# Performance work log

Hardware: AMD Instinct MI355X
Metric: run time of the kernel (lower is better)

Reference implementation:

```python
import jax, jax.numpy as jnp
import numpy as np

L = 3264          # seq_length
K = 12            # ktc=4 -> K=12
LOCC = 4          # ktc=4 -> Locc=4
BLK = 12          # mmse_block_size
DMIN, DMAX = -10, 10  # delay_search_range
RHO = 0.9         # assumed frequency-correlation coefficient for MMSE C matrix


def setup_inputs() -> dict:
    key = jax.random.key(0)
    k1, k2, k3 = jax.random.split(key, 3)
    ls_real = jax.random.normal(k1, (L,), dtype=jnp.float32)
    ls_imag = jax.random.normal(k2, (L,), dtype=jnp.float32)
    cyclic_shifts = jax.random.randint(k3, (8, 4), 0, K, dtype=jnp.int32)
    return {"ls_real": ls_real, "ls_imag": ls_imag, "cyclic_shifts": cyclic_shifts}


def _estimate(ls, cs_flat):
    P = cs_flat.shape[0]  # total ports across all users
    ideal = ((K - cs_flat) % K) * (L // K)                      # [P] ideal CIR peak positions
    h_time = jnp.fft.ifft(ls)
    hmag = jnp.abs(h_time)                                      # [L]
    idx = jnp.arange(L)
    # circular search window [ideal+DMIN, ideal+DMAX] around each ideal peak
    rel = (idx[None, :] - (ideal[:, None] + DMIN)) % L          # [P, L]
    mask = rel <= (DMAX - DMIN)
    vals = jnp.where(mask, hmag[None, :], -jnp.inf)
    peak = jnp.argmax(vals, axis=1)                             # [P]
    d = peak - ideal
    offset = jnp.where((peak > ideal) & (d > L // 2), d - L,
             jnp.where((ideal - peak) > L // 2, d + L, d))
    m = offset + ideal                                          # [P] phasor shift amounts
    # phasor exp(j 2 pi m n / L); reduce m*n mod L to keep fp32 phase accurate
    n = jnp.arange(L)
    phase = (2.0 * np.pi / L) * ((m[:, None] * n[None, :]) % L).astype(jnp.float32)
    phasor = jnp.exp(1j * phase).astype(jnp.complex64)          # [P, L]
    h_up = ls[None, :] * phasor                                 # [P, L]
    # OCC demux: average every LOCC points
    h_avg = h_up.reshape(P, L // LOCC, LOCC).mean(axis=-1)      # [P, L/LOCC]
    # linear interpolation back to L, centers of groups as sample points
    g = LOCC
    orig = (g - 1) / 2.0 + g * jnp.arange(L // g, dtype=jnp.float32)
    new = jnp.arange(L, dtype=jnp.float32)
    interp1 = jax.vmap(lambda r: jnp.interp(new, orig, r))
    h_interp = (interp1(jnp.real(h_avg)) + 1j * interp1(jnp.imag(h_avg))).astype(jnp.complex64)  # [P, L]
    # residual of multi-port reconstruction
    h_recon = jnp.sum(h_interp / phasor, axis=0)
    residual = ls - h_recon
    # noise power from adjacent-tone differences
    diff = ls[1:] - ls[:-1]
    noise_power = jnp.mean(jnp.abs(diff) ** 2) / 2.0
    # add residual back per port
    h_wr = h_interp + residual[None, :] * phasor                # [P, L]
    # block MMSE: h_mmse = C (C + noise I)^{-1} h_block, C[i,j] = rho^{|i-j|}
    ij = jnp.abs(jnp.arange(BLK)[:, None] - jnp.arange(BLK)[None, :])
    C = (RHO ** ij).astype(jnp.float32)
    A = C + noise_power * jnp.eye(BLK, dtype=jnp.float32)
    F = jnp.linalg.solve(A.T, C.T).T                            # F = C @ inv(A), [BLK, BLK]
    blocks = h_wr.reshape(P, L // BLK, BLK)
    h_mmse = jnp.einsum('pbk,jk->pbj', blocks, F.astype(jnp.complex64)).reshape(P, L)
    # the original nested loop emits the same P inner results for each of P outer (u,p)
    return jnp.tile(h_mmse, (P, 1))                             # [P*P, L]


def reference(ls_real, ls_imag, cyclic_shifts):
    ls = (ls_real + 1j * ls_imag).astype(jnp.complex64)
    cs_flat = cyclic_shifts.reshape(-1)
    return _estimate(ls, cs_flat)
```

## Files before the change

kernel.cpp:

```cpp
#include <hip/hip_runtime.h>
#include <math.h>

#define LL    3264
#define KK    12
#define PP    32
#define NW    21
#define DMIN  (-10)
#define GAVG  (LL/4)
#define NBLK  (LL/12)
#define NIDE  12
#define NMAG  (NIDE*NW)

#define OUT_REAL  (PP*PP*LL)
#define OUT_CPLX  (PP*PP*LL*2)
#define SCRATCH_F 270520

__global__ void k_win_noise_F(const float* __restrict__ lsr,
                              const float* __restrict__ lsi,
                              double* __restrict__ mag2,
                              float* __restrict__ F) {
    __shared__ double sre[256], sim[256];
    const int b = blockIdx.x;
    const int tid = threadIdx.x;
    const float c0 = (float)(2.0 * M_PI / (double)LL);
    if (b < NMAG) {
        const int i = b / NW, r = b % NW;
        int t = i * (LL / KK) + DMIN + r;
        t %= LL; if (t < 0) t += LL;
        double are = 0.0, aim = 0.0;
        for (int n = tid; n < LL; n += 256) {
            unsigned mod = (unsigned)(n * t) % LL;
            float ang = c0 * (float)mod;
            float ss, cc;
            sincosf(ang, &ss, &cc);
            float xr = lsr[n], xi = lsi[n];
            are += (double)(xr * cc - xi * ss);
            aim += (double)(xr * ss + xi * cc);
        }
        sre[tid] = are; sim[tid] = aim;
        __syncthreads();
        for (int s = 128; s > 0; s >>= 1) {
            if (tid < s) { sre[tid] += sre[tid + s]; sim[tid] += sim[tid + s]; }
            __syncthreads();
        }
        if (tid == 0) mag2[b] = sre[0] * sre[0] + sim[0] * sim[0];
    } else {
        double acc = 0.0;
        for (int n = tid; n < LL - 1; n += 256) {
            double dr = (double)lsr[n + 1] - (double)lsr[n];
            double di = (double)lsi[n + 1] - (double)lsi[n];
            acc += dr * dr + di * di;
        }
        sre[tid] = acc;
        __syncthreads();
        for (int s = 128; s > 0; s >>= 1) {
            if (tid < s) sre[tid] += sre[tid + s];
            __syncthreads();
        }
        if (tid == 0) sre[0] = (double)((float)(sre[0] / (double)(LL - 1) * 0.5));
        __syncthreads();
        const double npow = sre[0];

        __shared__ double A[12][12], Y[12][12];
        const int row = tid / 12, c = tid % 12;
        if (tid < 144) {
            int d = row - c; if (d < 0) d = -d;
            float cij = (float)pow(0.9, (double)d);
            A[row][c] = (double)cij + (row == c ? npow : 0.0);
            Y[row][c] = (double)cij;
        }
        __syncthreads();
        for (int col = 0; col < 12; col++) {
            double dinv = 0.0, pa = 0.0, py = 0.0, f = 0.0;
            if (tid < 144) {
                dinv = 1.0 / A[col][col];
                pa = A[col][c]; py = Y[col][c];
                f  = A[row][col];
            }
            __syncthreads();
            if (tid < 144) {
                if (row == col) { A[row][c] = pa * dinv; Y[row][c] = py * dinv; }
                else            { A[row][c] -= (f * dinv) * pa; Y[row][c] -= (f * dinv) * py; }
            }
            __syncthreads();
        }
        if (tid < 144) F[row * 12 + c] = (float)Y[c][row];
    }
}

template <bool CPLX>
__global__ __launch_bounds__(384) void k_fused(const float* __restrict__ lsr,
                                               const float* __restrict__ lsi,
                                               const int* __restrict__ cs,
                                               const double* __restrict__ mag2,
                                               const float* __restrict__ Fg,
                                               float* __restrict__ out) {
    const int b = blockIdx.x;
    const int tid = threadIdx.x;
    __shared__ float hav[32][5][2];
    __shared__ float hin[32][12][2];
    __shared__ float pha[32][12][2];
    __shared__ float con[32][12][2];
    __shared__ float w_s[32][12][2];
    __shared__ float res[12][2];
    __shared__ float Fs[144];
    __shared__ int   pk[32];
    __shared__ __align__(16) float smo[768];

    if (tid < 144) Fs[tid] = Fg[tid];
    if (tid < 32) {
        const int idl = (KK - cs[tid]) % KK;
        const int ideal = idl * (LL / KK);
        double best = -1.0; int bestl = 0x7fffffff;
        for (int r = 0; r < NW; r++) {
            int l = ideal + DMIN + r;
            l %= LL; if (l < 0) l += LL;
            double v = mag2[idl * NW + r];
            if (v > best || (v == best && l < bestl)) { best = v; bestl = l; }
        }
        pk[tid] = bestl;
    }
    __syncthreads();

    const int jb3 = 3 * b - 1;
    const int jbase = jb3 < 0 ? 0 : jb3;
    const float c0 = (float)(2.0 * M_PI / (double)LL);

    if (tid < 160) {
        const int p = tid / 5, js = tid % 5;
        int j = jbase + js; if (j > GAVG - 1) j = GAVG - 1;
        const int m = pk[p];
        float ar = 0.f, ai = 0.f;
        for (int s = 0; s < 4; s++) {
            int n = j * 4 + s;
            unsigned mod = (unsigned)(m * n) % LL;
            float ang = c0 * (float)mod;
            float ss, cc;
            sincosf(ang, &ss, &cc);
            float xr = lsr[n], xi = lsi[n];
            ar += xr * cc - xi * ss;
            ai += xr * ss + xi * cc;
        }
        hav[p][js][0] = ar * 0.25f;
        hav[p][js][1] = ai * 0.25f;
    }
    __syncthreads();

    {
        const int p = tid / 12, k = tid % 12;
        const int x = b * 12 + k;
        float re, im;
        if (x < 2)            { re = hav[p][0][0]; im = hav[p][0][1]; }
        else if (x >= LL - 2) { int js = (GAVG - 1) - jbase;
                                re = hav[p][js][0]; im = hav[p][js][1]; }
        else {
            int j = (x - 2) >> 2, js = j - jbase;
            float t = ((float)x - (1.5f + 4.0f * (float)j)) * 0.25f;
            float r0 = hav[p][js][0],     i0 = hav[p][js][1];
            float r1 = hav[p][js + 1][0], i1 = hav[p][js + 1][1];
            re = r0 + t * (r1 - r0);
            im = i0 + t * (i1 - i0);
        }
        hin[p][k][0] = re; hin[p][k][1] = im;
        const int m = pk[p];
        unsigned mod = (unsigned)(m * x) % LL;
        float ang = c0 * (float)mod;
        float ss, cc;
        sincosf(ang, &ss, &cc);
        pha[p][k][0] = cc; pha[p][k][1] = ss;
        float den = cc * cc + ss * ss;
        con[p][k][0] = (re * cc + im * ss) / den;
        con[p][k][1] = (im * cc - re * ss) / den;
    }
    __syncthreads();

    if (tid < 24) {
        const int k = tid >> 1, c = tid & 1;
        float s = 0.f;
        for (int p = 0; p < 32; p++) s += con[p][k][c];
        const int n = b * 12 + k;
        res[k][c] = (c ? lsi[n] : lsr[n]) - s;
    }
    __syncthreads();

    {
        const int p = tid / 12, k = tid % 12;
        float rr = res[k][0], ri = res[k][1];
        float cc = pha[p][k][0], ss = pha[p][k][1];
        w_s[p][k][0] = hin[p][k][0] + rr * cc - ri * ss;
        w_s[p][k][1] = hin[p][k][1] + rr * ss + ri * cc;
    }
    __syncthreads();

    {
        const int p = tid / 12, j = tid % 12;
        float ar = 0.f, ai = 0.f;
        for (int k = 0; k < 12; k++) {
            float f = Fs[j * 12 + k];
            ar += f * w_s[p][k][0];
            ai += f * w_s[p][k][1];
        }
        if (CPLX) { smo[(p * 12 + j) * 2] = ar; smo[(p * 12 + j) * 2 + 1] = ai; }
        else      { smo[p * 12 + j] = ar; }
    }
    __syncthreads();

    const float4* smo4 = (const float4*)smo;
    float4* out4 = (float4*)out;
    if (CPLX) {
        for (int idx = tid; idx < 32 * 192; idx += 384) {
            const int q = idx / 192, c = idx % 192;
            const int p = c / 6, w = c % 6;
            out4[(size_t)q * (PP * LL * 2 / 4) + p * (LL / 2) + b * 6 + w] = smo4[c];
        }
    } else {
        for (int idx = tid; idx < 32 * 96; idx += 384) {
            const int q = idx / 96, c = idx % 96;
            const int p = c / 3, w = c % 3;
            out4[(size_t)q * (PP * LL / 4) + p * (LL / 4) + b * 3 + w] = smo4[c];
        }
    }
}

__global__ void k_window_noise_fb(const float* __restrict__ lsr,
                                  const float* __restrict__ lsi,
                                  const int* __restrict__ cs,
                                  double* __restrict__ mag2,
                                  double* __restrict__ noise) {
    __shared__ double sre[256], sim[256];
    const int b = blockIdx.x;
    const int tid = threadIdx.x;
    const float c0 = (float)(2.0 * M_PI / (double)LL);
    if (b < PP * NW) {
        const int p = b / NW, r = b % NW;
        const int ideal = ((KK - cs[p]) % KK) * (LL / KK);
        int t = ideal + DMIN + r;
        t %= LL; if (t < 0) t += LL;
        double are = 0.0, aim = 0.0;
        for (int n = tid; n < LL; n += 256) {
            unsigned mod = (unsigned)(n * t) % LL;
            float ang = c0 * (float)mod;
            float ss, cc;
            sincosf(ang, &ss, &cc);
            float xr = lsr[n], xi = lsi[n];
            are += (double)(xr * cc - xi * ss);
            aim += (double)(xr * ss + xi * cc);
        }
        sre[tid] = are; sim[tid] = aim;
        __syncthreads();
        for (int s = 128; s > 0; s >>= 1) {
            if (tid < s) { sre[tid] += sre[tid + s]; sim[tid] += sim[tid + s]; }
            __syncthreads();
        }
        if (tid == 0) mag2[b] = sre[0] * sre[0] + sim[0] * sim[0];
    } else {
        double acc = 0.0;
        for (int n = tid; n < LL - 1; n += 256) {
            double dr = (double)lsr[n + 1] - (double)lsr[n];
            double di = (double)lsi[n + 1] - (double)lsi[n];
            acc += dr * dr + di * di;
        }
        sre[tid] = acc;
        __syncthreads();
        for (int s = 128; s > 0; s >>= 1) {
            if (tid < s) sre[tid] += sre[tid + s];
            __syncthreads();
        }
        if (tid == 0) *noise = sre[0] / (double)(LL - 1) * 0.5;
    }
}

__global__ void k_peak_F_fb(const int* __restrict__ cs,
                            const double* __restrict__ mag2,
                            const double* __restrict__ noise,
                            int* __restrict__ peak,
                            float* __restrict__ F) {
    __shared__ double A[12][12], Y[12][12];
    const int tid = threadIdx.x;
    if (tid < PP) {
        const int ideal = ((KK - cs[tid]) % KK) * (LL / KK);
        double best = -1.0; int bestl = 0x7fffffff;
        for (int r = 0; r < NW; r++) {
            int l = ideal + DMIN + r;
            l %= LL; if (l < 0) l += LL;
            double v = mag2[tid * NW + r];
            if (v > best || (v == best && l < bestl)) { best = v; bestl = l; }
        }
        peak[tid] = bestl;
    }
    const int row = tid / 12, c = tid % 12;
    if (tid < 144) {
        int d = row - c; if (d < 0) d = -d;
        float cij = (float)pow(0.9, (double)d);
        double npow = (double)((float)(*noise));
        A[row][c] = (double)cij + (row == c ? npow : 0.0);
        Y[row][c] = (double)cij;
    }
    __syncthreads();
    for (int col = 0; col < 12; col++) {
        double dinv = 0.0, pa = 0.0, py = 0.0, f = 0.0;
        if (tid < 144) {
            dinv = 1.0 / A[col][col];
            pa = A[col][c]; py = Y[col][c];
            f  = A[row][col];
        }
        __syncthreads();
        if (tid < 144) {
            if (row == col) { A[row][c] = pa * dinv; Y[row][c] = py * dinv; }
            else            { A[row][c] -= (f * dinv) * pa; Y[row][c] -= (f * dinv) * py; }
        }
        __syncthreads();
    }
    if (tid < 144) F[row * 12 + c] = (float)Y[c][row];
}

__global__ void k_havg(const float* __restrict__ lsr, const float* __restrict__ lsi,
                       const int* __restrict__ peak, float* __restrict__ havg) {
    const int idx = blockIdx.x * blockDim.x + threadIdx.x;
    if (idx >= PP * GAVG) return;
    const int p = idx / GAVG, jj = idx % GAVG;
    const int m = peak[p];
    const float c0 = (float)(2.0 * M_PI / (double)LL);
    float ar = 0.f, ai = 0.f;
    for (int s = 0; s < 4; s++) {
        int n = jj * 4 + s;
        unsigned mod = (unsigned)(m * n) % LL;
        float ph = c0 * (float)mod;
        float ss, cc;
        sincosf(ph, &ss, &cc);
        float xr = lsr[n], xi = lsi[n];
        ar += xr * cc - xi * ss;
        ai += xr * ss + xi * cc;
    }
    havg[idx * 2]     = ar * 0.25f;
    havg[idx * 2 + 1] = ai * 0.25f;
}

__global__ void k_interp(const float* __restrict__ havg, float* __restrict__ hinterp) {
    const int idx = blockIdx.x * blockDim.x + threadIdx.x;
    if (idx >= PP * LL) return;
    const int p = idx / LL, x = idx % LL;
    const float* hp = havg + (size_t)p * GAVG * 2;
    float re, im;
    if (x < 2) { re = hp[0]; im = hp[1]; }
    else if (x >= LL - 2) { re = hp[(GAVG - 1) * 2]; im = hp[(GAVG - 1) * 2 + 1]; }
    else {
        int j = (x - 2) >> 2;
        float t = ((float)x - (1.5f + 4.0f * (float)j)) * 0.25f;
        float r0 = hp[j * 2],       i0 = hp[j * 2 + 1];
        float r1 = hp[(j + 1) * 2], i1 = hp[(j + 1) * 2 + 1];
        re = r0 + t * (r1 - r0);
        im = i0 + t * (i1 - i0);
    }
    hinterp[idx * 2]     = re;
    hinterp[idx * 2 + 1] = im;
}

__global__ void k_resid(const float* __restrict__ lsr, const float* __restrict__ lsi,
                        const int* __restrict__ peak, const float* __restrict__ hinterp,
                        float* __restrict__ resid) {
    const int l = blockIdx.x * blockDim.x + threadIdx.x;
    if (l >= LL) return;
    const float c0 = (float)(2.0 * M_PI / (double)LL);
    float sr = 0.f, si = 0.f;
    for (int p = 0; p < PP; p++) {
        int m = peak[p];
        unsigned mod = (unsigned)(m * l) % LL;
        float ph = c0 * (float)mod;
        float ss, cc;
        sincosf(ph, &ss, &cc);
        float hr = hinterp[((size_t)p * LL + l) * 2];
        float hi = hinterp[((size_t)p * LL + l) * 2 + 1];
        float den = cc * cc + ss * ss;
        sr += (hr * cc + hi * ss) / den;
        si += (hi * cc - hr * ss) / den;
    }
    resid[l * 2]     = lsr[l] - sr;
    resid[l * 2 + 1] = lsi[l] - si;
}

template <bool CPLX>
__global__ void k_mmse(const int* __restrict__ peak, const float* __restrict__ hinterp,
                       const float* __restrict__ resid, const float* __restrict__ F,
                       float* __restrict__ out) {
    const int idx = blockIdx.x * blockDim.x + threadIdx.x;
    if (idx >= PP * NBLK) return;
    const int p = idx / NBLK, b = idx % NBLK;
    const int m = peak[p];
    const float c0 = (float)(2.0 * M_PI / (double)LL);
    float wr[12], wi[12];
    for (int k = 0; k < 12; k++) {
        int n = b * 12 + k;
        unsigned mod = (unsigned)(m * n) % LL;
        float ph = c0 * (float)mod;
        float ss, cc;
        sincosf(ph, &ss, &cc);
        float rr = resid[n * 2], ri = resid[n * 2 + 1];
        wr[k] = hinterp[((size_t)p * LL + n) * 2]     + (rr * cc - ri * ss);
        wi[k] = hinterp[((size_t)p * LL + n) * 2 + 1] + (rr * ss + ri * cc);
    }
    for (int j = 0; j < 12; j++) {
        float ar = 0.f, ai = 0.f;
        for (int k = 0; k < 12; k++) {
            float f = F[j * 12 + k];
            ar += f * wr[k];
            ai += f * wi[k];
        }
        if (CPLX) {
            float* orow = out + (size_t)p * LL * 2 + (size_t)b * 24;
            orow[j * 2]     = ar;
            orow[j * 2 + 1] = ai;
        } else {
            out[(size_t)p * LL + (size_t)b * 12 + j] = ar;
        }
    }
}

__global__ void k_tile(float4* __restrict__ out, int tile_f4) {
    const int idx = blockIdx.x * blockDim.x + threadIdx.x;
    if (idx >= tile_f4) return;
    float4 v = out[idx];
    for (int q = 1; q < PP; q++)
        out[(size_t)q * tile_f4 + idx] = v;
}

extern "C" void kernel_launch(void* const* d_in, const int* in_sizes, int n_in,
                              void* d_out, int out_size, void* d_ws, size_t ws_size,
                              hipStream_t stream) {
    const float* lsr = (const float*)d_in[0];
    const float* lsi = (const float*)d_in[1];
    const int*   cs  = (const int*)d_in[2];
    float* out = (float*)d_out;
    const bool cplx = (out_size >= OUT_CPLX);

    if (ws_size >= 16384) {
        double* mag2 = (double*)d_ws;
        float*  F    = (float*)(mag2 + NMAG);

        k_win_noise_F<<<NMAG + 1, 256, 0, stream>>>(lsr, lsi, mag2, F);
        if (cplx) k_fused<true ><<<NBLK, 384, 0, stream>>>(lsr, lsi, cs, mag2, F, out);
        else      k_fused<false><<<NBLK, 384, 0, stream>>>(lsr, lsi, cs, mag2, F, out);
    } else {
        float* base = out + ((size_t)out_size - SCRATCH_F);
        double* mag2  = (double*)base;
        double* noise = mag2 + PP * NW;
        int*    peak  = (int*)(base + 2692);
        float*  F     = base + 2724;
        float*  havg  = base + 2868;
        float*  hint  = base + 55092;
        float*  resid = base + 263988;

        k_window_noise_fb<<<PP * NW + 1, 256, 0, stream>>>(lsr, lsi, cs, mag2, noise);
        k_peak_F_fb<<<1, 192, 0, stream>>>(cs, mag2, noise, peak, F);
        k_havg<<<(PP * GAVG + 255) / 256, 256, 0, stream>>>(lsr, lsi, peak, havg);
        k_interp<<<(PP * LL + 255) / 256, 256, 0, stream>>>(havg, hint);
        k_resid<<<(LL + 255) / 256, 256, 0, stream>>>(lsr, lsi, peak, hint, resid);
        if (cplx) {
            k_mmse<true><<<(PP * NBLK + 255) / 256, 256, 0, stream>>>(peak, hint, resid, F, out);
            const int tile_f4 = PP * LL * 2 / 4;
            k_tile<<<(tile_f4 + 255) / 256, 256, 0, stream>>>((float4*)out, tile_f4);
        } else {
            k_mmse<false><<<(PP * NBLK + 255) / 256, 256, 0, stream>>>(peak, hint, resid, F, out);
            const int tile_f4 = PP * LL / 4;
            k_tile<<<(tile_f4 + 255) / 256, 256, 0, stream>>>((float4*)out, tile_f4);
        }
    }
}
```

Baseline: 26.50 us.

## Fuse window, noise and MMSE stages into one cooperative kernel with grid sync

Merges the window-magnitude/noise/F-solve kernel and the fused estimate kernel into a single cooperative launch, using a grid-wide sync in place of the kernel boundary. It also swaps shared-memory tree reductions for wavefront shuffle reductions. The aim is to remove one launch and its inter-kernel gap. The cost is a grid barrier across 272 blocks of 384 threads with the larger shared footprint, and a fallback to the old two-kernel path if the cooperative launch fails.

```diff
diff --git a/kernel.cpp b/kernel.cpp
--- a/kernel.cpp
+++ b/kernel.cpp
@@ -1,5 +1,8 @@
 #include <hip/hip_runtime.h>
+#include <hip/hip_cooperative_groups.h>
 #include <math.h>
+
+namespace cg = cooperative_groups;
 
 #define LL    3264
 #define KK    12
@@ -14,6 +17,217 @@
 #define OUT_REAL  (PP*PP*LL)
 #define OUT_CPLX  (PP*PP*LL*2)
 #define SCRATCH_F 270520
+
+__device__ __forceinline__ double wave_reduce(double v) {
+    for (int off = 32; off; off >>= 1) v += __shfl_down(v, off, 64);
+    return v;
+}
+
+template <bool CPLX>
+__global__ __launch_bounds__(384) void k_all(const float* __restrict__ lsr,
+                                             const float* __restrict__ lsi,
+                                             const int* __restrict__ cs,
+                                             double* __restrict__ mag2,
+                                             float* __restrict__ Fg,
+                                             float* __restrict__ out) {
+    const int b = blockIdx.x;
+    const int tid = threadIdx.x;
+    const float c0 = (float)(2.0 * M_PI / (double)LL);
+
+    __shared__ double sA[6], sB[6];
+    __shared__ double Amat[12][12], Ymat[12][12];
+    __shared__ float hav[32][5][2];
+    __shared__ float hin[32][12][2];
+    __shared__ float pha[32][12][2];
+    __shared__ float con[32][12][2];
+    __shared__ float w_s[32][12][2];
+    __shared__ float res[12][2];
+    __shared__ float Fs[144];
+    __shared__ int   pk[32];
+    __shared__ __align__(16) float smo[768];
+
+    if (b < NMAG) {
+        const int i = b / NW, r = b % NW;
+        int t = i * (LL / KK) + DMIN + r;
+        t %= LL; if (t < 0) t += LL;
+        double are = 0.0, aim = 0.0;
+        for (int n = tid; n < LL; n += 384) {
+            unsigned mod = (unsigned)(n * t) % LL;
+            float ang = c0 * (float)mod;
+            float ss, cc;
+            sincosf(ang, &ss, &cc);
+            float xr = lsr[n], xi = lsi[n];
+            are += (double)(xr * cc - xi * ss);
+            aim += (double)(xr * ss + xi * cc);
+        }
+        are = wave_reduce(are); aim = wave_reduce(aim);
+        const int wv = tid >> 6, ln = tid & 63;
+        if (ln == 0) { sA[wv] = are; sB[wv] = aim; }
+        __syncthreads();
+        if (tid == 0) {
+            double re = 0.0, im = 0.0;
+            for (int w = 0; w < 6; w++) { re += sA[w]; im += sB[w]; }
+            mag2[b] = re * re + im * im;
+        }
+    } else if (b == NMAG) {
+        double acc = 0.0;
+        for (int n = tid; n < LL - 1; n += 384) {
+            double dr = (double)lsr[n + 1] - (double)lsr[n];
+            double di = (double)lsi[n + 1] - (double)lsi[n];
+            acc += dr * dr + di * di;
+        }
+        acc = wave_reduce(acc);
+        const int wv = tid >> 6, ln = tid & 63;
+        if (ln == 0) sA[wv] = acc;
+        __syncthreads();
+        if (tid == 0) {
+            double s = 0.0;
+            for (int w = 0; w < 6; w++) s += sA[w];
+            sA[0] = (double)((float)(s / (double)(LL - 1) * 0.5));
+        }
+        __syncthreads();
+        const double npow = sA[0];
+        const int row = tid / 12, c = tid % 12;
+        if (tid < 144) {
+            int d = row - c; if (d < 0) d = -d;
+            float cij = (float)pow(0.9, (double)d);
+            Amat[row][c] = (double)cij + (row == c ? npow : 0.0);
+            Ymat[row][c] = (double)cij;
+        }
+        __syncthreads();
+        for (int col = 0; col < 12; col++) {
+            double dinv = 0.0, pa = 0.0, py = 0.0, f = 0.0;
+            if (tid < 144) {
+                dinv = 1.0 / Amat[col][col];
+                pa = Amat[col][c]; py = Ymat[col][c];
+                f  = Amat[row][col];
+            }
+            __syncthreads();
+            if (tid < 144) {
+                if (row == col) { Amat[row][c] = pa * dinv; Ymat[row][c] = py * dinv; }
+                else            { Amat[row][c] -= (f * dinv) * pa; Ymat[row][c] -= (f * dinv) * py; }
+            }
+            __syncthreads();
+        }
+        if (tid < 144) Fg[row * 12 + c] = (float)Ymat[c][row];
+    }
+
+    __threadfence();
+    cg::this_grid().sync();
+
+    if (tid < 144) Fs[tid] = Fg[tid];
+    if (tid < 32) {
+        const int idl = (KK - cs[tid]) % KK;
+        const int ideal = idl * (LL / KK);
+        double best = -1.0; int bestl = 0x7fffffff;
+        for (int r = 0; r < NW; r++) {
+            int l = ideal + DMIN + r;
+            l %= LL; if (l < 0) l += LL;
+            double v = mag2[idl * NW + r];
+            if (v > best || (v == best && l < bestl)) { best = v; bestl = l; }
+        }
+        pk[tid] = bestl;
+    }
+    __syncthreads();
+
+    const int jb3 = 3 * b - 1;
+    const int jbase = jb3 < 0 ? 0 : jb3;
+
+    if (tid < 160) {
+        const int p = tid / 5, js = tid % 5;
+        int j = jbase + js; if (j > GAVG - 1) j = GAVG - 1;
+        const int m = pk[p];
+        float ar = 0.f, ai = 0.f;
+        for (int s = 0; s < 4; s++) {
+            int n = j * 4 + s;
+            unsigned mod = (unsigned)(m * n) % LL;
+            float ang = c0 * (float)mod;
+            float ss, cc;
+            sincosf(ang, &ss, &cc);
+            float xr = lsr[n], xi = lsi[n];
+            ar += xr * cc - xi * ss;
+            ai += xr * ss + xi * cc;
+        }
+        hav[p][js][0] = ar * 0.25f;
+        hav[p][js][1] = ai * 0.25f;
+    }
+    __syncthreads();
+
+    {
+        const int p = tid / 12, k = tid % 12;
+        const int x = b * 12 + k;
+        float re, im;
+        if (x < 2)            { re = hav[p][0][0]; im = hav[p][0][1]; }
+        else if (x >= LL - 2) { int js = (GAVG - 1) - jbase;
+                                re = hav[p][js][0]; im = hav[p][js][1]; }
+        else {
+            int j = (x - 2) >> 2, js = j - jbase;
+            float t = ((float)x - (1.5f + 4.0f * (float)j)) * 0.25f;
+            float r0 = hav[p][js][0],     i0 = hav[p][js][1];
+            float r1 = hav[p][js + 1][0], i1 = hav[p][js + 1][1];
+            re = r0 + t * (r1 - r0);
+            im = i0 + t * (i1 - i0);
+        }
+        hin[p][k][0] = re; hin[p][k][1] = im;
+        const int m = pk[p];
+        unsigned mod = (unsigned)(m * x) % LL;
+        float ang = c0 * (float)mod;
+        float ss, cc;
+        sincosf(ang, &ss, &cc);
+        pha[p][k][0] = cc; pha[p][k][1] = ss;
+        float den = cc * cc + ss * ss;
+        con[p][k][0] = (re * cc + im * ss) / den;
+        con[p][k][1] = (im * cc - re * ss) / den;
+    }
+    __syncthreads();
+
+    if (tid < 24) {
+        const int k = tid >> 1, c = tid & 1;
+        float s = 0.f;
+        for (int p = 0; p < 32; p++) s += con[p][k][c];
+        const int n = b * 12 + k;
+        res[k][c] = (c ? lsi[n] : lsr[n]) - s;
+    }
+    __syncthreads();
+
+    {
+        const int p = tid / 12, k = tid % 12;
+        float rr = res[k][0], ri = res[k][1];
+        float cc = pha[p][k][0], ss = pha[p][k][1];
+        w_s[p][k][0] = hin[p][k][0] + rr * cc - ri * ss;
+        w_s[p][k][1] = hin[p][k][1] + rr * ss + ri * cc;
+    }
+    __syncthreads();
+
+    {
+        const int p = tid / 12, j = tid % 12;
+        float ar = 0.f, ai = 0.f;
+        for (int k = 0; k < 12; k++) {
+            float f = Fs[j * 12 + k];
+            ar += f * w_s[p][k][0];
+            ai += f * w_s[p][k][1];
+        }
+        if (CPLX) { smo[(p * 12 + j) * 2] = ar; smo[(p * 12 + j) * 2 + 1] = ai; }
+        else      { smo[p * 12 + j] = ar; }
+    }
+    __syncthreads();
+
+    const float4* smo4 = (const float4*)smo;
+    float4* out4 = (float4*)out;
+    if (CPLX) {
+        for (int idx = tid; idx < 32 * 192; idx += 384) {
+            const int q = idx / 192, c = idx % 192;
+            const int p = c / 6, w = c % 6;
+            out4[(size_t)q * (PP * LL * 2 / 4) + p * (LL / 2) + b * 6 + w] = smo4[c];
+        }
+    } else {
+        for (int idx = tid; idx < 32 * 96; idx += 384) {
+            const int q = idx / 96, c = idx % 96;
+            const int p = c / 3, w = c % 3;
+            out4[(size_t)q * (PP * LL / 4) + p * (LL / 4) + b * 3 + w] = smo4[c];
+        }
+    }
+}
 
 __global__ void k_win_noise_F(const float* __restrict__ lsr,
                               const float* __restrict__ lsi,
@@ -60,7 +274,6 @@
         if (tid == 0) sre[0] = (double)((float)(sre[0] / (double)(LL - 1) * 0.5));
         __syncthreads();
         const double npow = sre[0];
-
         __shared__ double A[12][12], Y[12][12];
         const int row = tid / 12, c = tid % 12;
         if (tid < 144) {
@@ -437,9 +650,22 @@
         double* mag2 = (double*)d_ws;
         float*  F    = (float*)(mag2 + NMAG);
 
-        k_win_noise_F<<<NMAG + 1, 256, 0, stream>>>(lsr, lsi, mag2, F);
-        if (cplx) k_fused<true ><<<NBLK, 384, 0, stream>>>(lsr, lsi, cs, mag2, F, out);
-        else      k_fused<false><<<NBLK, 384, 0, stream>>>(lsr, lsi, cs, mag2, F, out);
+        void* args[6];
+        args[0] = (void*)&lsr; args[1] = (void*)&lsi; args[2] = (void*)&cs;
+        args[3] = (void*)&mag2; args[4] = (void*)&F; args[5] = (void*)&out;
+        hipError_t err;
+        if (cplx)
+            err = hipLaunchCooperativeKernel((const void*)k_all<true>,
+                                             dim3(NBLK), dim3(384), args, 0, stream);
+        else
+            err = hipLaunchCooperativeKernel((const void*)k_all<false>,
+                                             dim3(NBLK), dim3(384), args, 0, stream);
+
+        if (err != hipSuccess) {
+            k_win_noise_F<<<NMAG + 1, 256, 0, stream>>>(lsr, lsi, mag2, F);
+            if (cplx) k_fused<true ><<<NBLK, 384, 0, stream>>>(lsr, lsi, cs, mag2, F, out);
+            else      k_fused<false><<<NBLK, 384, 0, stream>>>(lsr, lsi, cs, mag2, F, out);
+        }
     } else {
         float* base = out + ((size_t)out_size - SCRATCH_F);
         double* mag2  = (double*)base;
```

Measured after the change: 96.80 us. 3.65x slower.

## Process four MMSE blocks per workgroup in fused estimation kernel

Applied to the files above, without the earlier changes.

The fused kernel now gives each workgroup 48 subcarriers (four 12-wide MMSE blocks) instead of 12, launching a quarter as many workgroups. This amortises the per-block setup (F load, peak search over mag2, synchronisation) and widens the contiguous float4 output stores per row. Shared buffers are reused (hin holds the residual-corrected values, con is reused as the output staging area) to keep LDS usage down. The trade-off is fewer workgroups (68), which may underfill the GPU's compute units while the output write dominates.

```diff
diff --git a/kernel.cpp b/kernel.cpp
--- a/kernel.cpp
+++ b/kernel.cpp
@@ -8,6 +8,9 @@
 #define DMIN  (-10)
 #define GAVG  (LL/4)
 #define NBLK  (LL/12)
+#define NB    4
+#define NBLK4 (NBLK/NB)
+#define NSLOT 14
 #define NIDE  12
 #define NMAG  (NIDE*NW)
 
@@ -60,7 +63,6 @@
         if (tid == 0) sre[0] = (double)((float)(sre[0] / (double)(LL - 1) * 0.5));
         __syncthreads();
         const double npow = sre[0];
-
         __shared__ double A[12][12], Y[12][12];
         const int row = tid / 12, c = tid % 12;
         if (tid < 144) {
@@ -89,23 +91,24 @@
 }
 
 template <bool CPLX>
-__global__ __launch_bounds__(384) void k_fused(const float* __restrict__ lsr,
-                                               const float* __restrict__ lsi,
-                                               const int* __restrict__ cs,
-                                               const double* __restrict__ mag2,
-                                               const float* __restrict__ Fg,
-                                               float* __restrict__ out) {
-    const int b = blockIdx.x;
+__global__ __launch_bounds__(384) void k_fused4(const float* __restrict__ lsr,
+                                                const float* __restrict__ lsi,
+                                                const int* __restrict__ cs,
+                                                const double* __restrict__ mag2,
+                                                const float* __restrict__ Fg,
+                                                float* __restrict__ out) {
+    const int bb = blockIdx.x;
     const int tid = threadIdx.x;
-    __shared__ float hav[32][5][2];
-    __shared__ float hin[32][12][2];
-    __shared__ float pha[32][12][2];
-    __shared__ float con[32][12][2];
-    __shared__ float w_s[32][12][2];
-    __shared__ float res[12][2];
+    const int x0 = bb * (12 * NB);
+    const float c0 = (float)(2.0 * M_PI / (double)LL);
+
+    __shared__ float hav[32][NSLOT][2];
+    __shared__ __align__(16) float hin[32][48][2];
+    __shared__ float pha[32][48][2];
+    __shared__ __align__(16) float con[32][48][2];
+    __shared__ float res[48][2];
     __shared__ float Fs[144];
     __shared__ int   pk[32];
-    __shared__ __align__(16) float smo[768];
 
     if (tid < 144) Fs[tid] = Fg[tid];
     if (tid < 32) {
@@ -122,12 +125,11 @@
     }
     __syncthreads();
 
-    const int jb3 = 3 * b - 1;
-    const int jbase = jb3 < 0 ? 0 : jb3;
-    const float c0 = (float)(2.0 * M_PI / (double)LL);
-
-    if (tid < 160) {
-        const int p = tid / 5, js = tid % 5;
+    const int jb = 12 * bb - 1;
+    const int jbase = jb < 0 ? 0 : jb;
+
+    for (int it = tid; it < 32 * NSLOT; it += 384) {
+        const int p = it / NSLOT, js = it % NSLOT;
         int j = jbase + js; if (j > GAVG - 1) j = GAVG - 1;
         const int m = pk[p];
         float ar = 0.f, ai = 0.f;
@@ -146,9 +148,9 @@
     }
     __syncthreads();
 
-    {
-        const int p = tid / 12, k = tid % 12;
-        const int x = b * 12 + k;
+    for (int it = tid; it < 32 * 48; it += 384) {
+        const int p = it / 48, xl = it % 48;
+        const int x = x0 + xl;
         float re, im;
         if (x < 2)            { re = hav[p][0][0]; im = hav[p][0][1]; }
         else if (x >= LL - 2) { int js = (GAVG - 1) - jbase;
@@ -161,63 +163,66 @@
             re = r0 + t * (r1 - r0);
             im = i0 + t * (i1 - i0);
         }
-        hin[p][k][0] = re; hin[p][k][1] = im;
+        hin[p][xl][0] = re; hin[p][xl][1] = im;
         const int m = pk[p];
         unsigned mod = (unsigned)(m * x) % LL;
         float ang = c0 * (float)mod;
         float ss, cc;
         sincosf(ang, &ss, &cc);
-        pha[p][k][0] = cc; pha[p][k][1] = ss;
+        pha[p][xl][0] = cc; pha[p][xl][1] = ss;
         float den = cc * cc + ss * ss;
-        con[p][k][0] = (re * cc + im * ss) / den;
-        con[p][k][1] = (im * cc - re * ss) / den;
-    }
-    __syncthreads();
-
-    if (tid < 24) {
-        const int k = tid >> 1, c = tid & 1;
+        con[p][xl][0] = (re * cc + im * ss) / den;
+        con[p][xl][1] = (im * cc - re * ss) / den;
+    }
+    __syncthreads();
+
+    if (tid < 96) {
+        const int xl = tid >> 1, c = tid & 1;
         float s = 0.f;
-        for (int p = 0; p < 32; p++) s += con[p][k][c];
-        const int n = b * 12 + k;
-        res[k][c] = (c ? lsi[n] : lsr[n]) - s;
-    }
-    __syncthreads();
-
-    {
-        const int p = tid / 12, k = tid % 12;
-        float rr = res[k][0], ri = res[k][1];
-        float cc = pha[p][k][0], ss = pha[p][k][1];
-        w_s[p][k][0] = hin[p][k][0] + rr * cc - ri * ss;
-        w_s[p][k][1] = hin[p][k][1] + rr * ss + ri * cc;
-    }
-    __syncthreads();
-
-    {
-        const int p = tid / 12, j = tid % 12;
+        for (int p = 0; p < 32; p++) s += con[p][xl][c];
+        const int n = x0 + xl;
+        res[xl][c] = (c ? lsi[n] : lsr[n]) - s;
+    }
+    __syncthreads();
+
+    for (int it = tid; it < 32 * 48; it += 384) {
+        const int p = it / 48, xl = it % 48;
+        float rr = res[xl][0], ri = res[xl][1];
+        float cc = pha[p][xl][0], ss = pha[p][xl][1];
+        float wr = hin[p][xl][0] + rr * cc - ri * ss;
+        float wi = hin[p][xl][1] + rr * ss + ri * cc;
+        hin[p][xl][0] = wr; hin[p][xl][1] = wi;
+    }
+    __syncthreads();
+
+    float* smo = &con[0][0][0];
+    for (int it = tid; it < 32 * 48; it += 384) {
+        const int p = it / 48, xl = it % 48;
+        const int bi = xl / 12, j = xl % 12;
         float ar = 0.f, ai = 0.f;
         for (int k = 0; k < 12; k++) {
             float f = Fs[j * 12 + k];
-            ar += f * w_s[p][k][0];
-            ai += f * w_s[p][k][1];
-        }
-        if (CPLX) { smo[(p * 12 + j) * 2] = ar; smo[(p * 12 + j) * 2 + 1] = ai; }
-        else      { smo[p * 12 + j] = ar; }
+            ar += f * hin[p][bi * 12 + k][0];
+            ai += f * hin[p][bi * 12 + k][1];
+        }
+        if (CPLX) { smo[(p * 48 + xl) * 2] = ar; smo[(p * 48 + xl) * 2 + 1] = ai; }
+        else      { smo[p * 48 + xl] = ar; }
     }
     __syncthreads();
 
     const float4* smo4 = (const float4*)smo;
     float4* out4 = (float4*)out;
     if (CPLX) {
-        for (int idx = tid; idx < 32 * 192; idx += 384) {
-            const int q = idx / 192, c = idx % 192;
-            const int p = c / 6, w = c % 6;
-            out4[(size_t)q * (PP * LL * 2 / 4) + p * (LL / 2) + b * 6 + w] = smo4[c];
+        for (int idx = tid; idx < 32 * 768; idx += 384) {
+            const int q = idx / 768, c = idx % 768;
+            const int p = c / 24, w = c % 24;
+            out4[(size_t)q * (PP * LL * 2 / 4) + p * (LL / 2) + bb * 24 + w] = smo4[c];
         }
     } else {
-        for (int idx = tid; idx < 32 * 96; idx += 384) {
-            const int q = idx / 96, c = idx % 96;
-            const int p = c / 3, w = c % 3;
-            out4[(size_t)q * (PP * LL / 4) + p * (LL / 4) + b * 3 + w] = smo4[c];
+        for (int idx = tid; idx < 32 * 384; idx += 384) {
+            const int q = idx / 384, c = idx % 384;
+            const int p = c / 12, w = c % 12;
+            out4[(size_t)q * (PP * LL / 4) + p * (LL / 4) + bb * 12 + w] = smo4[c];
         }
     }
 }
@@ -438,8 +443,8 @@
         float*  F    = (float*)(mag2 + NMAG);
 
         k_win_noise_F<<<NMAG + 1, 256, 0, stream>>>(lsr, lsi, mag2, F);
-        if (cplx) k_fused<true ><<<NBLK, 384, 0, stream>>>(lsr, lsi, cs, mag2, F, out);
-        else      k_fused<false><<<NBLK, 384, 0, stream>>>(lsr, lsi, cs, mag2, F, out);
+        if (cplx) k_fused4<true ><<<NBLK4, 384, 0, stream>>>(lsr, lsi, cs, mag2, F, out);
+        else      k_fused4<false><<<NBLK4, 384, 0, stream>>>(lsr, lsi, cs, mag2, F, out);
     } else {
         float* base = out + ((size_t)out_size - SCRATCH_F);
         double* mag2  = (double*)base;
```

New measurement: 24.77 us. -6.5%, faster.
